# Kernel optimization log

Measured on AMD Instinct MI355X. Metric: run time of the kernel, lower is better.

Reference implementation:

```python
import jax, jax.numpy as jnp
import numpy as np

N_QUBITS = 8
N_LAYERS = 4


def setup_inputs() -> dict:
    key = jax.random.key(0)
    k_x, k_rot, k_ent, k_w, k_b = jax.random.split(key, 5)
    B, S, F = 64, 8192, 64
    x = jax.random.normal(k_x, (B, S, F), dtype=jnp.float32)
    rotation_params = jax.random.normal(k_rot, (N_LAYERS, N_QUBITS, 3), dtype=jnp.float32) * 0.01
    entangle_params = jax.random.normal(k_ent, (N_LAYERS, N_QUBITS - 1), dtype=jnp.float32) * 0.01
    proj_w = jax.random.normal(k_w, (N_QUBITS * 2, N_QUBITS), dtype=jnp.float32) * (1.0 / np.sqrt(N_QUBITS))
    proj_b = jax.random.normal(k_b, (N_QUBITS * 2,), dtype=jnp.float32) * 0.01
    return {"x": x, "rotation_params": rotation_params, "entangle_params": entangle_params,
            "proj_w": proj_w, "proj_b": proj_b}


def reference(x, rotation_params, entangle_params, proj_w, proj_b):
    n_layers, n_qubits, _ = rotation_params.shape
    # amplitude encoding: tanh of first n_qubits features -> [B, S, Q]
    qs = jnp.tanh(x[..., :n_qubits])
    for layer in range(n_layers):
        r = rotation_params[layer]  # [Q, 3]
        # rx, ry, rz are each (cos+sin)*state -> fused per-qubit scale
        scale = ((jnp.cos(r[:, 0]) + jnp.sin(r[:, 0]))
                 * (jnp.cos(r[:, 1]) + jnp.sin(r[:, 1]))
                 * (jnp.cos(r[:, 2]) + jnp.sin(r[:, 2])))  # [Q]
        rz = qs * scale  # broadcast over [B, S, Q]
        # entanglement: entangled[..., i] = rz[i]*(1-w_i) + rz[i+1]*w_i, last qubit unchanged
        w = jax.nn.sigmoid(entangle_params[layer])  # [Q-1]
        front = rz[..., :-1] * (1.0 - w) + rz[..., 1:] * w
        qs = jnp.concatenate([front, rz[..., -1:]], axis=-1)
    # projection Linear(Q -> 2Q)
    return jnp.einsum('bsq,oq->bso', qs, proj_w) + proj_b
```

## Files before the change

kernel.cpp:

```cpp
#include <hip/hip_runtime.h>

#define NQ 8
#define NL 4
#define NO 16

typedef __attribute__((ext_vector_type(4))) float float4v;

__global__ __launch_bounds__(256) void qcl_fused(
    const float* __restrict__ x,
    const float* __restrict__ rot,
    const float* __restrict__ ent,
    const float* __restrict__ pw,
    const float* __restrict__ pb,
    float* __restrict__ out,
    int n_rows)
{
    __shared__ float sW[NO][NQ];
    __shared__ float sB[NO];
    const int tid = threadIdx.x;

    if (tid < NO) {
        float W[NQ];
        #pragma unroll
        for (int q = 0; q < NQ; ++q) W[q] = pw[tid * NQ + q];

        #pragma unroll
        for (int l = NL - 1; l >= 0; --l) {
            float wl[NQ - 1];
            #pragma unroll
            for (int i = 0; i < NQ - 1; ++i) {
                float e = __expf(-ent[l * (NQ - 1) + i]);
                wl[i] = __builtin_amdgcn_rcpf(1.0f + e);
            }
            float WE[NQ];
            WE[0] = W[0] * (1.0f - wl[0]);
            #pragma unroll
            for (int j = 1; j < NQ - 1; ++j)
                WE[j] = W[j] * (1.0f - wl[j]) + W[j - 1] * wl[j - 1];
            WE[NQ - 1] = W[NQ - 1] + W[NQ - 2] * wl[NQ - 2];
            #pragma unroll
            for (int q = 0; q < NQ; ++q) {
                float r0 = rot[(l * NQ + q) * 3 + 0];
                float r1 = rot[(l * NQ + q) * 3 + 1];
                float r2 = rot[(l * NQ + q) * 3 + 2];
                float s = (__cosf(r0) + __sinf(r0)) *
                          (__cosf(r1) + __sinf(r1)) *
                          (__cosf(r2) + __sinf(r2));
                W[q] = WE[q] * s;
            }
        }
        #pragma unroll
        for (int q = 0; q < NQ; ++q) sW[tid][q] = W[q];
        sB[tid] = pb[tid];
    }
    __syncthreads();

    const int nhalf = n_rows * 2;
    const int H = gridDim.x * 256;
    const int gid = blockIdx.x * 256 + tid;
    const int h = tid & 1;

    const int g0 = gid;
    const int g1 = gid + H;
    const bool v0 = g0 < nhalf;
    const bool v1 = g1 < nhalf;

    float4v a0 = {0.f, 0.f, 0.f, 0.f};
    float4v a1 = {0.f, 0.f, 0.f, 0.f};
    if (v0) a0 = *(const float4v*)(x + (size_t)(g0 >> 1) * 64 + h * 4);
    if (v1) a1 = *(const float4v*)(x + (size_t)(g1 >> 1) * 64 + h * 4);

    float m0[4], m1[4];
    #pragma unroll
    for (int j = 0; j < 4; ++j) {
        float e0 = __expf(2.0f * a0[j]);
        m0[j] = 1.0f - 2.0f * __builtin_amdgcn_rcpf(e0 + 1.0f);
        float e1 = __expf(2.0f * a1[j]);
        m1[j] = 1.0f - 2.0f * __builtin_amdgcn_rcpf(e1 + 1.0f);
    }

    float tA[8], tB[8];
    #pragma unroll
    for (int j = 0; j < 4; ++j) {
        float o0 = __shfl_xor(m0[j], 1, 64);
        float o1 = __shfl_xor(m1[j], 1, 64);
        tA[j]     = h ? o0 : m0[j];
        tA[j + 4] = h ? m0[j] : o0;
        tB[j]     = h ? o1 : m1[j];
        tB[j + 4] = h ? m1[j] : o1;
    }

    const int base = h * 8;
    float accA[8], accB[8];
    #pragma unroll
    for (int j = 0; j < 8; ++j) {
        float aA = sB[base + j];
        float aB = aA;
        #pragma unroll
        for (int q = 0; q < NQ; ++q) {
            float w = sW[base + j][q];
            aA += w * tA[q];
            aB += w * tB[q];
        }
        accA[j] = aA;
        accB[j] = aB;
    }

    if (v0) {
        float4v* p = (float4v*)(out + (size_t)(g0 >> 1) * 16 + base);
        float4v u0 = {accA[0], accA[1], accA[2], accA[3]};
        float4v u1 = {accA[4], accA[5], accA[6], accA[7]};
        p[0] = u0; p[1] = u1;
    }
    if (v1) {
        float4v* p = (float4v*)(out + (size_t)(g1 >> 1) * 16 + base);
        float4v u0 = {accB[0], accB[1], accB[2], accB[3]};
        float4v u1 = {accB[4], accB[5], accB[6], accB[7]};
        p[0] = u0; p[1] = u1;
    }
}

extern "C" void kernel_launch(void* const* d_in, const int* in_sizes, int n_in,
                              void* d_out, int out_size, void* d_ws, size_t ws_size,
                              hipStream_t stream) {
    const float* x   = (const float*)d_in[0];
    const float* rot = (const float*)d_in[1];
    const float* ent = (const float*)d_in[2];
    const float* pw  = (const float*)d_in[3];
    const float* pb  = (const float*)d_in[4];
    float* out = (float*)d_out;

    const int n_rows = in_sizes[0] / 64;
    const int nhalf = n_rows * 2;
    const int block = 256;
    const int grid = (nhalf + block * 2 - 1) / (block * 2);
    hipLaunchKernelGGL(qcl_fused, dim3(grid), dim3(block), 0, stream,
                       x, rot, ent, pw, pb, out, n_rows);
}
```

Before: 27.35 us.

## Parallelize weight folding across threads, issue x loads first, nontemporal output stores

Issues the global loads of x before the per-block weight folding so their latency overlaps the setup work. The sin/cos scales and sigmoid weights are now computed in parallel by separate threads and staged in shared memory, instead of serially by 16 threads, at the cost of an extra barrier. The projection now reads weight rows as float4 vectors from LDS. Output writes become nontemporal stores to avoid polluting the cache.

New measurement: 26.12 us, median of 2. -4.5%, faster.

```diff
diff --git a/kernel.cpp b/kernel.cpp
--- a/kernel.cpp
+++ b/kernel.cpp
@@ -15,51 +15,17 @@
     float* __restrict__ out,
     int n_rows)
 {
+    __shared__ float sScale[NL][NQ];
+    __shared__ float sWl[NL][NQ - 1];
     __shared__ float sW[NO][NQ];
     __shared__ float sB[NO];
+
     const int tid = threadIdx.x;
-
-    if (tid < NO) {
-        float W[NQ];
-        #pragma unroll
-        for (int q = 0; q < NQ; ++q) W[q] = pw[tid * NQ + q];
-
-        #pragma unroll
-        for (int l = NL - 1; l >= 0; --l) {
-            float wl[NQ - 1];
-            #pragma unroll
-            for (int i = 0; i < NQ - 1; ++i) {
-                float e = __expf(-ent[l * (NQ - 1) + i]);
-                wl[i] = __builtin_amdgcn_rcpf(1.0f + e);
-            }
-            float WE[NQ];
-            WE[0] = W[0] * (1.0f - wl[0]);
-            #pragma unroll
-            for (int j = 1; j < NQ - 1; ++j)
-                WE[j] = W[j] * (1.0f - wl[j]) + W[j - 1] * wl[j - 1];
-            WE[NQ - 1] = W[NQ - 1] + W[NQ - 2] * wl[NQ - 2];
-            #pragma unroll
-            for (int q = 0; q < NQ; ++q) {
-                float r0 = rot[(l * NQ + q) * 3 + 0];
-                float r1 = rot[(l * NQ + q) * 3 + 1];
-                float r2 = rot[(l * NQ + q) * 3 + 2];
-                float s = (__cosf(r0) + __sinf(r0)) *
-                          (__cosf(r1) + __sinf(r1)) *
-                          (__cosf(r2) + __sinf(r2));
-                W[q] = WE[q] * s;
-            }
-        }
-        #pragma unroll
-        for (int q = 0; q < NQ; ++q) sW[tid][q] = W[q];
-        sB[tid] = pb[tid];
-    }
-    __syncthreads();
 
     const int nhalf = n_rows * 2;
     const int H = gridDim.x * 256;
     const int gid = blockIdx.x * 256 + tid;
     const int h = tid & 1;
-
     const int g0 = gid;
     const int g1 = gid + H;
     const bool v0 = g0 < nhalf;
@@ -69,6 +35,46 @@
     float4v a1 = {0.f, 0.f, 0.f, 0.f};
     if (v0) a0 = *(const float4v*)(x + (size_t)(g0 >> 1) * 64 + h * 4);
     if (v1) a1 = *(const float4v*)(x + (size_t)(g1 >> 1) * 64 + h * 4);
+
+    if (tid < NL * NQ) {
+        const int l = tid >> 3, q = tid & 7;
+        const float r0 = rot[(l * NQ + q) * 3 + 0];
+        const float r1 = rot[(l * NQ + q) * 3 + 1];
+        const float r2 = rot[(l * NQ + q) * 3 + 2];
+        sScale[l][q] = (__cosf(r0) + __sinf(r0)) *
+                       (__cosf(r1) + __sinf(r1)) *
+                       (__cosf(r2) + __sinf(r2));
+    } else if (tid < NL * NQ + NL * (NQ - 1)) {
+        const int u = tid - NL * NQ;
+        const int l = u / 7, i = u - l * 7;
+        const float e = __expf(-ent[l * 7 + i]);
+        sWl[l][i] = __builtin_amdgcn_rcpf(1.0f + e);
+    } else if (tid >= 64 && tid < 64 + NO) {
+        sB[tid - 64] = pb[tid - 64];
+    }
+    __syncthreads();
+
+    if (tid < NO) {
+        float W[NQ];
+        #pragma unroll
+        for (int q = 0; q < NQ; ++q) W[q] = pw[tid * NQ + q];
+        #pragma unroll
+        for (int l = NL - 1; l >= 0; --l) {
+            float WE[NQ];
+            WE[0] = W[0] * (1.0f - sWl[l][0]);
+            #pragma unroll
+            for (int j = 1; j < NQ - 1; ++j)
+                WE[j] = W[j] * (1.0f - sWl[l][j]) + W[j - 1] * sWl[l][j - 1];
+            WE[NQ - 1] = W[NQ - 1] + W[NQ - 2] * sWl[l][NQ - 2];
+            #pragma unroll
+            for (int q = 0; q < NQ; ++q) W[q] = WE[q] * sScale[l][q];
+        }
+        #pragma unroll
+        for (int q = 0; q < NQ; ++q) sW[tid][q] = W[q];
+    }
+    __syncthreads();
+
+    if (!v0 && !v1) return;
 
     float m0[4], m1[4];
     #pragma unroll
@@ -91,32 +97,32 @@
     }
 
     const int base = h * 8;
+    const float4v* wrow = (const float4v*)&sW[base][0];
     float accA[8], accB[8];
     #pragma unroll
     for (int j = 0; j < 8; ++j) {
-        float aA = sB[base + j];
-        float aB = aA;
-        #pragma unroll
-        for (int q = 0; q < NQ; ++q) {
-            float w = sW[base + j][q];
-            aA += w * tA[q];
-            aB += w * tB[q];
-        }
-        accA[j] = aA;
-        accB[j] = aB;
+        float4v w0 = wrow[2 * j];
+        float4v w1 = wrow[2 * j + 1];
+        float bj = sB[base + j];
+        accA[j] = bj + w0.x * tA[0] + w0.y * tA[1] + w0.z * tA[2] + w0.w * tA[3]
+                     + w1.x * tA[4] + w1.y * tA[5] + w1.z * tA[6] + w1.w * tA[7];
+        accB[j] = bj + w0.x * tB[0] + w0.y * tB[1] + w0.z * tB[2] + w0.w * tB[3]
+                     + w1.x * tB[4] + w1.y * tB[5] + w1.z * tB[6] + w1.w * tB[7];
     }
 
     if (v0) {
         float4v* p = (float4v*)(out + (size_t)(g0 >> 1) * 16 + base);
         float4v u0 = {accA[0], accA[1], accA[2], accA[3]};
         float4v u1 = {accA[4], accA[5], accA[6], accA[7]};
-        p[0] = u0; p[1] = u1;
+        __builtin_nontemporal_store(u0, p);
+        __builtin_nontemporal_store(u1, p + 1);
     }
     if (v1) {
         float4v* p = (float4v*)(out + (size_t)(g1 >> 1) * 16 + base);
         float4v u0 = {accB[0], accB[1], accB[2], accB[3]};
         float4v u1 = {accB[4], accB[5], accB[6], accB[7]};
-        p[0] = u0; p[1] = u1;
+        __builtin_nontemporal_store(u0, p);
+        __builtin_nontemporal_store(u1, p + 1);
     }
 }
 
```
